# Performance work log

Hardware: AMD Instinct MI355X
Metric: run time of the kernel (lower is better)

## Reference

```python
import jax, jax.numpy as jnp
import numpy as np

N_CHILDS = 50000
N_EDGES = 500000
NODE_FEAT = 256
NUM_SEM = 57
HID = 256
EDGE_FEAT = 64
EDGE_TYPES = 4
NUM_ITERS = 2


def setup_inputs() -> dict:
    key = jax.random.key(0)
    ks = jax.random.split(key, 12)
    d_in = NODE_FEAT + NUM_SEM            # 313
    d_ne = 2 * HID + EDGE_FEAT + EDGE_TYPES  # 580
    d_par = HID * (NUM_ITERS + 1)         # 768
    def lin(k, fan_in, fan_out):
        kw, kb = jax.random.split(k)
        s = 1.0 / np.sqrt(fan_in)
        return (jax.random.uniform(kw, (fan_in, fan_out), jnp.float32, -s, s),
                jax.random.uniform(kb, (fan_out,), jnp.float32, -s, s))
    W_child, b_child = lin(ks[0], d_in, HID)
    W_ne0, b_ne0 = lin(ks[1], d_ne, HID)
    W_ne1, b_ne1 = lin(ks[2], d_ne, HID)
    W_parent, b_parent = lin(ks[3], d_par, NODE_FEAT)
    return {
        "child_feats": jax.random.normal(ks[4], (1, N_CHILDS, d_in), jnp.float32),
        "child_exists": jnp.ones((1, N_CHILDS, 1), jnp.float32),
        "edge_type_onehot": jax.random.normal(ks[5], (1, N_EDGES, EDGE_TYPES), jnp.float32),
        "edge_feats": jax.random.normal(ks[6], (1, N_EDGES, EDGE_FEAT), jnp.float32),
        "edge_indices": jax.random.randint(ks[7], (1, N_EDGES, 2), 0, N_CHILDS, jnp.int64),
        "W_child": W_child, "b_child": b_child,
        "W_ne0": W_ne0, "b_ne0": b_ne0,
        "W_ne1": W_ne1, "b_ne1": b_ne1,
        "W_parent": W_parent, "b_parent": b_parent,
    }


def reference(child_feats, child_exists, edge_type_onehot, edge_feats, edge_indices,
              W_child, b_child, W_ne0, b_ne0, W_ne1, b_ne1, W_parent, b_parent):
    n = child_feats.shape[1]
    # node embedding: linear + relu, mask non-existent children
    x = jax.nn.relu(jnp.einsum('bnd,dh->bnh', child_feats, W_child) + b_child)
    x = x * child_exists                              # [1, N, H]
    iter_parent = [x.max(axis=1)]                     # symmetric_type == 'max'
    ef = jnp.concatenate([edge_type_onehot, edge_feats], axis=2)[0]  # [E, 4+64]
    src = edge_indices[0, :, 0]
    dst = edge_indices[0, :, 1]
    cnt = jax.ops.segment_sum(jnp.ones((src.shape[0],), x.dtype), src, num_segments=n)
    denom = jnp.maximum(cnt, 1.0)[:, None]            # scatter_mean clamp
    for W, b in ((W_ne0, b_ne0), (W_ne1, b_ne1)):
        nef = jnp.concatenate([x[0, src], x[0, dst], ef], axis=1)  # [E, 580]
        nef = jax.nn.relu(nef @ W + b)                # [E, H]
        # edge_symmetric_type == 'avg': scatter_mean over source index
        x = (jax.ops.segment_sum(nef, src, num_segments=n) / denom)[None]
        iter_parent.append(x.max(axis=1))
    parent = jnp.concatenate(iter_parent, axis=1)     # [1, H*(iters+1)]
    return jax.nn.relu(parent @ W_parent + b_parent)  # [1, node_feat_size]
```

## Files before the change

### kernel.cpp

```cpp
#include <hip/hip_runtime.h>

#define NC   50000
#define NE   500000
#define NEP  (NE + 64)
#define DIN  313
#define DNE  580
#define KPC  320
#define KB   96
#define NB_SCAN 196

typedef __attribute__((ext_vector_type(8))) short bf16x8;
typedef __attribute__((ext_vector_type(4))) float f32x4;

static __device__ __forceinline__ unsigned short f2bf(float f) {
    unsigned u = __float_as_uint(f);
    unsigned r = (u + 0x7fff + ((u >> 16) & 1)) >> 16;
    return (unsigned short)r;
}
static __device__ __forceinline__ float bf2f(unsigned short u) {
    return __uint_as_float(((unsigned)u) << 16);
}
static __device__ __forceinline__ void gload_lds16(const unsigned short* g, unsigned short* l) {
    __builtin_amdgcn_global_load_lds(
        (const __attribute__((address_space(1))) unsigned int*)(g),
        (__attribute__((address_space(3))) unsigned int*)(l), 16, 0, 0);
}

__global__ __launch_bounds__(256) void prep_w_kernel(
    const float* __restrict__ W0, const float* __restrict__ W1,
    const float* __restrict__ Wc,
    unsigned short* __restrict__ Wpt, unsigned short* __restrict__ Wbt,
    unsigned short* __restrict__ Wct)
{
    int b = blockIdx.x;
    if (b < 1024) {
        int layer = b >> 9, n2 = b & 511;
        const float* W = layer ? W1 : W0;
        unsigned short* dst = Wpt + (size_t)layer * 512 * 256 + (size_t)n2 * 256;
        int t = threadIdx.x;
        int ch = t >> 5, s = (t >> 3) & 3, j = t & 7;
        int gk = ch * 32 + ((s ^ (n2 & 3)) * 8) + j;
        float v = (n2 < 256) ? W[(size_t)gk * 256 + n2] : W[(size_t)(256 + gk) * 256 + (n2 - 256)];
        dst[t] = f2bf(v);
    } else if (b < 1536) {
        int idx = b - 1024;
        int layer = idx >> 8, n = idx & 255;
        const float* W = layer ? W1 : W0;
        unsigned short* dst = Wbt + (size_t)layer * 256 * KB + (size_t)n * KB;
        int t = threadIdx.x;
        if (t < KB) {
            int ch = t >> 5, s = (t >> 3) & 3, j = t & 7;
            int gk = ch * 32 + ((s ^ (n & 3)) * 8) + j;
            float v = (512 + gk < DNE) ? W[(size_t)(512 + gk) * 256 + n] : 0.0f;
            dst[t] = f2bf(v);
        }
    } else {
        int n = b - 1536;
        unsigned short* dst = Wct + (size_t)n * KPC;
        for (int t = threadIdx.x; t < KPC; t += 256) {
            int ch = t >> 5, s = (t >> 3) & 3, j = t & 7;
            int gk = ch * 32 + ((s ^ (n & 3)) * 8) + j;
            float v = (gk < DIN) ? Wc[(size_t)gk * 256 + n] : 0.0f;
            dst[t] = f2bf(v);
        }
    }
}

__global__ __launch_bounds__(256, 4) void child_mfma_kernel(
    const float* __restrict__ cf, const float* __restrict__ exists,
    const unsigned short* __restrict__ Wct, const float* __restrict__ bias,
    unsigned short* __restrict__ xb, float* __restrict__ pmax)
{
    __shared__ unsigned short sA[64][40];
    __shared__ unsigned short sB[256][32];
    __shared__ float smax[256];

    const int tid = threadIdx.x, lane = tid & 63, wid = tid >> 6;
    const int wm = wid >> 1, wn = wid & 1, l15 = lane & 15, l4 = lane >> 4;
    const int node0 = blockIdx.x * 64;
    const int arow = tid >> 2, s3 = tid & 3;

    smax[tid] = 0.0f;

    f32x4 acc[2][8];
    #pragma unroll
    for (int mi = 0; mi < 2; ++mi)
        #pragma unroll
        for (int ni = 0; ni < 8; ++ni)
            acc[mi][ni] = (f32x4){0.f, 0.f, 0.f, 0.f};

    int nodeA = node0 + arow; if (nodeA >= NC) nodeA = NC - 1;

    for (int ch = 0; ch < 10; ++ch) {
        #pragma unroll
        for (int i = 0; i < 4; ++i) {
            int n = (wid << 6) + (i << 4) + (lane >> 2);
            gload_lds16(Wct + (size_t)n * KPC + ch * 32 + (lane & 3) * 8,
                        &sB[(wid << 6) + (i << 4)][0]);
        }
        {
            int gk0 = ch * 32 + s3 * 8;
            union { unsigned short u[8]; int4 v; } pk;
            #pragma unroll
            for (int j = 0; j < 8; ++j) {
                int gk = gk0 + j;
                float f = (gk < DIN) ? cf[(size_t)nodeA * DIN + gk] : 0.0f;
                pk.u[j] = f2bf(f);
            }
            *(int4*)&sA[arow][s3 * 8] = pk.v;
        }
        __syncthreads();
        bf16x8 af[2];
        #pragma unroll
        for (int mi = 0; mi < 2; ++mi)
            af[mi] = *(const bf16x8*)&sA[wm * 32 + mi * 16 + l15][l4 * 8];
        #pragma unroll
        for (int ni = 0; ni < 8; ++ni) {
            int n = wn * 128 + ni * 16 + l15;
            bf16x8 bfr = *(const bf16x8*)&sB[n][(l4 ^ (n & 3)) * 8];
            acc[0][ni] = __builtin_amdgcn_mfma_f32_16x16x32_bf16(af[0], bfr, acc[0][ni], 0, 0, 0);
            acc[1][ni] = __builtin_amdgcn_mfma_f32_16x16x32_bf16(af[1], bfr, acc[1][ni], 0, 0, 0);
        }
        __syncthreads();
    }

    float bv[8];
    #pragma unroll
    for (int ni = 0; ni < 8; ++ni) bv[ni] = bias[wn * 128 + ni * 16 + l15];
    float cmax[8];
    #pragma unroll
    for (int ni = 0; ni < 8; ++ni) cmax[ni] = 0.0f;

    #pragma unroll
    for (int mi = 0; mi < 2; ++mi) {
        #pragma unroll
        for (int r = 0; r < 4; ++r) {
            int node = node0 + wm * 32 + mi * 16 + l4 * 4 + r;
            if (node < NC) {
                float ex = exists[node];
                #pragma unroll
                for (int ni = 0; ni < 8; ++ni) {
                    float v = fmaxf(acc[mi][ni][r] + bv[ni], 0.f) * ex;
                    xb[(size_t)node * 256 + wn * 128 + ni * 16 + l15] = f2bf(v);
                    cmax[ni] = fmaxf(cmax[ni], v);
                }
            }
        }
    }
    #pragma unroll
    for (int ni = 0; ni < 8; ++ni)
        atomicMax((unsigned int*)&smax[wn * 128 + ni * 16 + l15], __float_as_uint(cmax[ni]));
    __syncthreads();
    atomicMax((unsigned int*)&pmax[tid], __float_as_uint(smax[tid]));
}

__global__ __launch_bounds__(256, 3) void node_gemm_kernel(
    const unsigned short* __restrict__ xb,
    const unsigned short* __restrict__ Wpt,
    unsigned short* __restrict__ yp)
{
    __shared__ unsigned short sA[2][64][40];
    __shared__ unsigned short sB[2][256][32];

    const int tid = threadIdx.x, lane = tid & 63, wid = tid >> 6;
    const int wm = wid >> 1, wn = wid & 1, l15 = lane & 15, l4 = lane >> 4;
    const int node0 = blockIdx.x * 64;
    const int n0 = blockIdx.y * 256;
    const int arow = tid >> 2, s3 = tid & 3;

    int nodeA = node0 + arow; if (nodeA >= NC) nodeA = NC - 1;

    f32x4 acc[2][8];
    #pragma unroll
    for (int mi = 0; mi < 2; ++mi)
        #pragma unroll
        for (int ni = 0; ni < 8; ++ni)
            acc[mi][ni] = (f32x4){0.f, 0.f, 0.f, 0.f};

    #pragma unroll
    for (int i = 0; i < 4; ++i) {
        int n = (wid << 6) + (i << 4) + (lane >> 2);
        gload_lds16(Wpt + (size_t)(n0 + n) * 256 + (lane & 3) * 8, &sB[0][(wid << 6) + (i << 4)][0]);
    }
    *(int4*)&sA[0][arow][s3 * 8] = *(const int4*)(xb + (size_t)nodeA * 256 + s3 * 8);
    __syncthreads();

    int buf = 0;
    for (int ch = 0; ch < 8; ++ch) {
        const int nch = ch + 1;
        int4 areg;
        if (nch < 8) {
            #pragma unroll
            for (int i = 0; i < 4; ++i) {
                int n = (wid << 6) + (i << 4) + (lane >> 2);
                gload_lds16(Wpt + (size_t)(n0 + n) * 256 + nch * 32 + (lane & 3) * 8,
                            &sB[buf ^ 1][(wid << 6) + (i << 4)][0]);
            }
            areg = *(const int4*)(xb + (size_t)nodeA * 256 + nch * 32 + s3 * 8);
        }
        bf16x8 af[2];
        #pragma unroll
        for (int mi = 0; mi < 2; ++mi)
            af[mi] = *(const bf16x8*)&sA[buf][wm * 32 + mi * 16 + l15][l4 * 8];
        #pragma unroll
        for (int ni = 0; ni < 8; ++ni) {
            int n = wn * 128 + ni * 16 + l15;
            bf16x8 bfr = *(const bf16x8*)&sB[buf][n][(l4 ^ (n & 3)) * 8];
            acc[0][ni] = __builtin_amdgcn_mfma_f32_16x16x32_bf16(af[0], bfr, acc[0][ni], 0, 0, 0);
            acc[1][ni] = __builtin_amdgcn_mfma_f32_16x16x32_bf16(af[1], bfr, acc[1][ni], 0, 0, 0);
        }
        if (nch < 8) *(int4*)&sA[buf ^ 1][arow][s3 * 8] = areg;
        __syncthreads();
        buf ^= 1;
    }

    #pragma unroll
    for (int mi = 0; mi < 2; ++mi) {
        #pragma unroll
        for (int r = 0; r < 4; ++r) {
            int node = node0 + wm * 32 + mi * 16 + l4 * 4 + r;
            if (node < NC) {
                #pragma unroll
                for (int ni = 0; ni < 8; ++ni)
                    yp[(size_t)node * 512 + n0 + wn * 128 + ni * 16 + l15] = f2bf(acc[mi][ni][r]);
            }
        }
    }
}

__global__ __launch_bounds__(256) void count_int_kernel(
    const int* __restrict__ eidx, int* __restrict__ icnt)
{
    int t = blockIdx.x * 256 + threadIdx.x;
    if (t < NE) atomicAdd(&icnt[eidx[2 * t]], 1);
}

__global__ __launch_bounds__(256) void scan1_kernel(
    const int* __restrict__ icnt, int* __restrict__ part)
{
    __shared__ int sd[256];
    int i = blockIdx.x * 256 + threadIdx.x;
    sd[threadIdx.x] = (i < NC) ? icnt[i] : 0;
    __syncthreads();
    for (int d = 128; d > 0; d >>= 1) {
        if (threadIdx.x < d) sd[threadIdx.x] += sd[threadIdx.x + d];
        __syncthreads();
    }
    if (threadIdx.x == 0) part[blockIdx.x] = sd[0];
}

__global__ void scan2_kernel(int* __restrict__ part)
{
    if (threadIdx.x == 0) {
        int acc = 0;
        for (int i = 0; i < NB_SCAN; ++i) { int v = part[i]; part[i] = acc; acc += v; }
    }
}

__global__ __launch_bounds__(256) void scan3_kernel(
    const int* __restrict__ icnt, const int* __restrict__ part,
    int* __restrict__ cur)
{
    __shared__ int sc[256];
    const int t = threadIdx.x;
    int i = blockIdx.x * 256 + t;
    int val = (i < NC) ? icnt[i] : 0;
    sc[t] = val;
    __syncthreads();
    for (int d = 1; d < 256; d <<= 1) {
        int x = (t >= d) ? sc[t - d] : 0;
        __syncthreads();
        sc[t] += x;
        __syncthreads();
    }
    if (i < NC) cur[i] = part[blockIdx.x] + sc[t] - val;
}

__global__ __launch_bounds__(256) void bin_kernel(
    const int* __restrict__ eidx, int* __restrict__ cur, int* __restrict__ perm)
{
    int t = blockIdx.x * 256 + threadIdx.x;
    if (t < NE) {
        int s = eidx[2 * t];
        int p = atomicAdd(&cur[s], 1);
        perm[p] = t;
    }
}

__global__ __launch_bounds__(256) void inv_kernel(
    const int* __restrict__ icnt, float* __restrict__ inv)
{
    int t = blockIdx.x * 256 + threadIdx.x;
    if (t < NC) inv[t] = 1.0f / fmaxf((float)icnt[t], 1.0f);
}

__global__ __launch_bounds__(256) void ef_prep_kernel(
    const float* __restrict__ eto, const float* __restrict__ efe,
    const int* __restrict__ perm, const int* __restrict__ eidx,
    unsigned short* __restrict__ efc01, unsigned short* __restrict__ efc2,
    int* __restrict__ esrc, int* __restrict__ edst)
{
    int p = blockIdx.x * 256 + threadIdx.x;
    if (p >= NE) return;
    int e = perm[p];
    esrc[p] = eidx[2 * e];
    edst[p] = eidx[2 * e + 1];
    const float* efr = efe + (size_t)e * 64;

    union { unsigned short u[8]; int4 v; } pk;
    {
        float4 a = *(const float4*)(eto + (size_t)e * 4);
        float4 b = *(const float4*)(efr + 0);
        pk.u[0]=f2bf(a.x); pk.u[1]=f2bf(a.y); pk.u[2]=f2bf(a.z); pk.u[3]=f2bf(a.w);
        pk.u[4]=f2bf(b.x); pk.u[5]=f2bf(b.y); pk.u[6]=f2bf(b.z); pk.u[7]=f2bf(b.w);
        *(int4*)(efc01 + (size_t)p * 32) = pk.v;
    }
    #pragma unroll
    for (int g = 1; g < 4; ++g) {
        float4 a = *(const float4*)(efr + g * 8 - 4);
        float4 b = *(const float4*)(efr + g * 8);
        pk.u[0]=f2bf(a.x); pk.u[1]=f2bf(a.y); pk.u[2]=f2bf(a.z); pk.u[3]=f2bf(a.w);
        pk.u[4]=f2bf(b.x); pk.u[5]=f2bf(b.y); pk.u[6]=f2bf(b.z); pk.u[7]=f2bf(b.w);
        *(int4*)(efc01 + (size_t)p * 32 + g * 8) = pk.v;
    }
    #pragma unroll
    for (int g = 0; g < 4; ++g) {
        float4 a = *(const float4*)(efr + 28 + g * 8);
        float4 b = *(const float4*)(efr + 32 + g * 8);
        pk.u[0]=f2bf(a.x); pk.u[1]=f2bf(a.y); pk.u[2]=f2bf(a.z); pk.u[3]=f2bf(a.w);
        pk.u[4]=f2bf(b.x); pk.u[5]=f2bf(b.y); pk.u[6]=f2bf(b.z); pk.u[7]=f2bf(b.w);
        *(int4*)(efc01 + ((size_t)NEP + p) * 32 + g * 8) = pk.v;
    }
    {
        float4 a = *(const float4*)(efr + 60);
        pk.u[0]=f2bf(a.x); pk.u[1]=f2bf(a.y); pk.u[2]=f2bf(a.z); pk.u[3]=f2bf(a.w);
        pk.u[4]=0; pk.u[5]=0; pk.u[6]=0; pk.u[7]=0;
        *(int4*)(efc2 + (size_t)p * 8) = pk.v;
    }
}

__global__ __launch_bounds__(256, 3) void combine_efc_kernel(
    const unsigned short* __restrict__ yp,
    const unsigned short* __restrict__ efc01,
    const unsigned short* __restrict__ efc2,
    const int* __restrict__ esrc, const int* __restrict__ edst,
    const unsigned short* __restrict__ Wbt,
    const float* __restrict__ bias,
    float* __restrict__ accb)
{
    __shared__ __align__(16) unsigned char smem[25600];
    unsigned short (*sA01)[64][32] = (unsigned short (*)[64][32])(smem);
    unsigned short (*sA2)[8]       = (unsigned short (*)[8])(smem + 8192);
    unsigned short (*sW)[32]       = (unsigned short (*)[32])(smem + 9216);
    float (*ep)[258]               = (float (*)[258])(smem);
    __shared__ int s_src[64], s_dst[64];

    const int tid = threadIdx.x;
    const int nwg = gridDim.x;
    const int q = nwg >> 3, rr = nwg & 7;
    const int xcd = blockIdx.x & 7, within = blockIdx.x >> 3;
    const int bid = (xcd < rr ? xcd * (q + 1) : rr * (q + 1) + (xcd - rr) * q) + within;
    const int e0 = bid * 64;

    const int lane = tid & 63;
    const int wid  = tid >> 6;
    const int wm   = wid >> 1;
    const int wn   = wid & 1;
    const int l15  = lane & 15;
    const int l4   = lane >> 4;

    if (tid < 64) {
        int e = e0 + tid; if (e > NE - 1) e = NE - 1;
        s_src[tid] = esrc[e];
        s_dst[tid] = edst[e];
    }
    gload_lds16(efc01 + ((size_t)e0 + wid * 16) * 32 + lane * 8, &sA01[0][wid * 16][0]);
    gload_lds16(efc01 + ((size_t)NEP + e0 + wid * 16) * 32 + lane * 8, &sA01[1][wid * 16][0]);
    if (wid == 0)
        gload_lds16(efc2 + (size_t)e0 * 8 + lane * 8, &sA2[0][0]);
    #pragma unroll
    for (int i = 0; i < 4; ++i) {
        gload_lds16(Wbt + (size_t)((wid << 6) + (i << 4) + (lane >> 2)) * KB + (lane & 3) * 8,
                    &sW[(wid << 6) + (i << 4)][0]);
    }
    __syncthreads();

    f32x4 acc[2][8];
    #pragma unroll
    for (int mi = 0; mi < 2; ++mi)
        #pragma unroll
        for (int ni = 0; ni < 8; ++ni)
            acc[mi][ni] = (f32x4){0.f, 0.f, 0.f, 0.f};

    #pragma unroll
    for (int ch = 0; ch < 3; ++ch) {
        if (ch > 0) {
            __syncthreads();
            #pragma unroll
            for (int i = 0; i < 4; ++i) {
                gload_lds16(Wbt + (size_t)((wid << 6) + (i << 4) + (lane >> 2)) * KB + ch * 32 + (lane & 3) * 8,
                            &sW[(wid << 6) + (i << 4)][0]);
            }
            __syncthreads();
        }
        bf16x8 af0, af1;
        if (ch < 2) {
            af0 = *(const bf16x8*)&sA01[ch][wm * 32 + l15][l4 * 8];
            af1 = *(const bf16x8*)&sA01[ch][wm * 32 + 16 + l15][l4 * 8];
        } else {
            bf16x8 z = (bf16x8){0,0,0,0,0,0,0,0};
            bf16x8 a0 = *(const bf16x8*)&sA2[wm * 32 + l15][0];
            bf16x8 a1 = *(const bf16x8*)&sA2[wm * 32 + 16 + l15][0];
            af0 = (l4 == 0) ? a0 : z;
            af1 = (l4 == 0) ? a1 : z;
        }
        #pragma unroll
        for (int ni = 0; ni < 8; ++ni) {
            int n = wn * 128 + ni * 16 + l15;
            bf16x8 bfr = *(const bf16x8*)&sW[n][(l4 ^ (n & 3)) * 8];
            acc[0][ni] = __builtin_amdgcn_mfma_f32_16x16x32_bf16(af0, bfr, acc[0][ni], 0, 0, 0);
            acc[1][ni] = __builtin_amdgcn_mfma_f32_16x16x32_bf16(af1, bfr, acc[1][ni], 0, 0, 0);
        }
    }
    __syncthreads();

    const int col = tid;
    const float b_col = bias[col];

    int curn = s_src[0];
    int rstart = 0;
    float run = 0.f;
    #pragma unroll
    for (int c = 0; c < 4; ++c) {
        if (wm == (c >> 1)) {
            const int mi = c & 1;
            #pragma unroll
            for (int ni = 0; ni < 8; ++ni) {
                #pragma unroll
                for (int r = 0; r < 4; ++r)
                    ep[l4 * 4 + r][wn * 128 + ni * 16 + l15] = acc[mi][ni][r];
            }
        }
        float yt[16], ym[16];
        #pragma unroll
        for (int r = 0; r < 16; ++r) {
            int row = c * 16 + r;
            yt[r] = bf2f(yp[(size_t)s_src[row] * 512 + col]);
            ym[r] = bf2f(yp[(size_t)s_dst[row] * 512 + 256 + col]);
        }
        __syncthreads();
        #pragma unroll
        for (int r = 0; r < 16; ++r) {
            int row = c * 16 + r;
            float v = 0.0f;
            if (e0 + row < NE)
                v = fmaxf(ep[r][col] + yt[r] + ym[r] + b_col, 0.f);
            int sr = s_src[row];
            if (sr != curn) {
                if (rstart > 0) accb[(size_t)curn * 256 + col] = run;
                else            atomicAdd(&accb[(size_t)curn * 256 + col], run);
                curn = sr; run = v; rstart = row;
            } else {
                run += v;
            }
        }
        __syncthreads();
    }
    atomicAdd(&accb[(size_t)curn * 256 + col], run);
}

__global__ __launch_bounds__(256, 3) void combine_f32_kernel(
    const unsigned short* __restrict__ yp,
    const float* __restrict__ eto, const float* __restrict__ efe,
    const int* __restrict__ eidx, const int* __restrict__ perm,
    const unsigned short* __restrict__ Wbt,
    const float* __restrict__ bias,
    float* __restrict__ accb)
{
    __shared__ unsigned short sA[3][64][40];
    __shared__ unsigned short sW[2][256][32];
    __shared__ int s_src[64], s_dst[64], s_perm[64];

    const int tid = threadIdx.x;
    const int nwg = gridDim.x;
    const int q = nwg >> 3, rr = nwg & 7;
    const int xcd = blockIdx.x & 7, within = blockIdx.x >> 3;
    const int bid = (xcd < rr ? xcd * (q + 1) : rr * (q + 1) + (xcd - rr) * q) + within;
    const int e0 = bid * 64;

    if (tid < 64) {
        int ee = e0 + tid; if (ee >= NE) ee = NE - 1;
        int e = perm[ee];
        s_perm[tid] = e;
        s_src[tid] = eidx[2 * e];
        s_dst[tid] = eidx[2 * e + 1];
    }
    const int lane = tid & 63;
    const int wid  = tid >> 6;
    const int wm   = wid >> 1;
    const int wn   = wid & 1;
    const int l15  = lane & 15;
    const int l4   = lane >> 4;
    const int arow = tid >> 2;
    const int s3   = tid & 3;

    f32x4 acc[2][8];
    #pragma unroll
    for (int mi = 0; mi < 2; ++mi)
        #pragma unroll
        for (int ni = 0; ni < 8; ++ni)
            acc[mi][ni] = (f32x4){0.f, 0.f, 0.f, 0.f};

    #pragma unroll
    for (int i = 0; i < 4; ++i) {
        int n = (wid << 6) + (i << 4) + (lane >> 2);
        gload_lds16(Wbt + (size_t)n * KB + (lane & 3) * 8, &sW[0][(wid << 6) + (i << 4)][0]);
    }
    __syncthreads();

    const int my_e = s_perm[arow];
    #pragma unroll
    for (int ch = 0; ch < 3; ++ch) {
        int g0 = ch * 32 + s3 * 8;
        union { unsigned short u[8]; int4 v; } pk;
        #pragma unroll
        for (int j = 0; j < 8; ++j) {
            int g = g0 + j;
            float f = 0.0f;
            if (g < 4)       f = eto[(size_t)my_e * 4 + g];
            else if (g < 68) f = efe[(size_t)my_e * 64 + (g - 4)];
            pk.u[j] = f2bf(f);
        }
        *(int4*)&sA[ch][arow][s3 * 8] = pk.v;
    }
    __syncthreads();

    int buf = 0;
    #pragma unroll
    for (int ch = 0; ch < 3; ++ch) {
        if (ch + 1 < 3) {
            #pragma unroll
            for (int i = 0; i < 4; ++i) {
                int n = (wid << 6) + (i << 4) + (lane >> 2);
                gload_lds16(Wbt + (size_t)n * KB + (ch + 1) * 32 + (lane & 3) * 8,
                            &sW[buf ^ 1][(wid << 6) + (i << 4)][0]);
            }
        }
        bf16x8 af[2];
        #pragma unroll
        for (int mi = 0; mi < 2; ++mi)
            af[mi] = *(const bf16x8*)&sA[ch][wm * 32 + mi * 16 + l15][l4 * 8];
        #pragma unroll
        for (int ni = 0; ni < 8; ++ni) {
            int n = wn * 128 + ni * 16 + l15;
            bf16x8 bfr = *(const bf16x8*)&sW[buf][n][(l4 ^ (n & 3)) * 8];
            acc[0][ni] = __builtin_amdgcn_mfma_f32_16x16x32_bf16(af[0], bfr, acc[0][ni], 0, 0, 0);
            acc[1][ni] = __builtin_amdgcn_mfma_f32_16x16x32_bf16(af[1], bfr, acc[1][ni], 0, 0, 0);
        }
        __syncthreads();
        buf ^= 1;
    }

    float (*ep)[258] = (float (*)[258])(&sW[0][0][0]);
    const int col = tid;
    const float b_col = bias[col];

    int curn = s_src[0];
    int rstart = 0;
    float run = 0.f;
    #pragma unroll
    for (int c = 0; c < 4; ++c) {
        if (wm == (c >> 1)) {
            const int mi = c & 1;
            #pragma unroll
            for (int ni = 0; ni < 8; ++ni) {
                #pragma unroll
                for (int r = 0; r < 4; ++r)
                    ep[l4 * 4 + r][wn * 128 + ni * 16 + l15] = acc[mi][ni][r];
            }
        }
        float yt[16], ym[16];
        #pragma unroll
        for (int r = 0; r < 16; ++r) {
            int row = c * 16 + r;
            yt[r] = bf2f(yp[(size_t)s_src[row] * 512 + col]);
            ym[r] = bf2f(yp[(size_t)s_dst[row] * 512 + 256 + col]);
        }
        __syncthreads();
        #pragma unroll
        for (int r = 0; r < 16; ++r) {
            int row = c * 16 + r;
            float v = 0.0f;
            if (e0 + row < NE)
                v = fmaxf(ep[r][col] + yt[r] + ym[r] + b_col, 0.f);
            int sr = s_src[row];
            if (sr != curn) {
                if (rstart > 0) accb[(size_t)curn * 256 + col] = run;
                else            atomicAdd(&accb[(size_t)curn * 256 + col], run);
                curn = sr; run = v; rstart = row;
            } else {
                run += v;
            }
        }
        __syncthreads();
    }
    atomicAdd(&accb[(size_t)curn * 256 + col], run);
}

__global__ __launch_bounds__(256) void finalize_kernel(
    const float* __restrict__ src, const float* __restrict__ inv,
    unsigned short* __restrict__ xb_out, float* __restrict__ pmax, int n)
{
    const int tid = threadIdx.x;
    int i0 = blockIdx.x * 128;
    int iend = i0 + 128; if (iend > n) iend = n;
    float m = 0.0f;
    for (int i = i0; i < iend; ++i) {
        float v = src[(size_t)i * 256 + tid];
        v *= inv[i];
        xb_out[(size_t)i * 256 + tid] = f2bf(v);
        m = fmaxf(m, v);
    }
    atomicMax((unsigned int*)&pmax[tid], __float_as_uint(m));
}

__global__ __launch_bounds__(256) void parent_kernel(
    const float* __restrict__ pmax, const float* __restrict__ W,
    const float* __restrict__ bias, float* __restrict__ out)
{
    __shared__ float sp[768];
    const int tid = threadIdx.x;
    for (int i = tid; i < 768; i += 256) sp[i] = pmax[i];
    __syncthreads();
    float s = bias[tid];
    for (int k = 0; k < 768; ++k) s = fmaf(sp[k], W[(size_t)k * 256 + tid], s);
    out[tid] = fmaxf(s, 0.f);
}

extern "C" void kernel_launch(void* const* d_in, const int* in_sizes, int n_in,
                              void* d_out, int out_size, void* d_ws, size_t ws_size,
                              hipStream_t stream)
{
    const float* cf   = (const float*)d_in[0];
    const float* ex   = (const float*)d_in[1];
    const float* eto  = (const float*)d_in[2];
    const float* efe  = (const float*)d_in[3];
    const int*   eidx = (const int*)d_in[4];
    const float* Wc   = (const float*)d_in[5];
    const float* bc   = (const float*)d_in[6];
    const float* W0   = (const float*)d_in[7];
    const float* b0   = (const float*)d_in[8];
    const float* W1   = (const float*)d_in[9];
    const float* b1   = (const float*)d_in[10];
    const float* Wp   = (const float*)d_in[11];
    const float* bp   = (const float*)d_in[12];

    float*          accb = (float*)d_ws;
    float*          invv = accb + (size_t)NC * 256;
    float*          pmax = invv + NC;
    unsigned short* xb   = (unsigned short*)(pmax + 768);
    unsigned short* yp   = xb + (size_t)NC * 256;
    unsigned short* Wpt  = yp + (size_t)NC * 512;
    unsigned short* Wbt  = Wpt + (size_t)2 * 512 * 256;
    unsigned short* Wct  = Wbt + (size_t)2 * 256 * KB;
    int*            icnt = (int*)(Wct + (size_t)256 * KPC);
    int*            part = icnt + NC;
    int*            curb = part + 256;
    int*            perm = curb + NC;
    unsigned short* efc01 = (unsigned short*)(perm + NE);
    unsigned short* efc2  = efc01 + (size_t)2 * NEP * 32;
    int*            esrc  = (int*)(efc2 + (size_t)NEP * 8);
    int*            edst  = esrc + NE;
    size_t need = (size_t)((char*)(edst + NE) - (char*)d_ws);
    const bool use_efc = (ws_size >= need);

    hipMemsetAsync(pmax, 0, 768 * sizeof(float), stream);
    hipMemsetAsync(icnt, 0, NC * sizeof(int), stream);

    prep_w_kernel<<<1792, 256, 0, stream>>>(W0, W1, Wc, Wpt, Wbt, Wct);
    child_mfma_kernel<<<(NC + 63) / 64, 256, 0, stream>>>(cf, ex, Wct, bc, xb, pmax);

    count_int_kernel<<<(NE + 255) / 256, 256, 0, stream>>>(eidx, icnt);
    scan1_kernel<<<NB_SCAN, 256, 0, stream>>>(icnt, part);
    scan2_kernel<<<1, 64, 0, stream>>>(part);
    scan3_kernel<<<NB_SCAN, 256, 0, stream>>>(icnt, part, curb);
    bin_kernel<<<(NE + 255) / 256, 256, 0, stream>>>(eidx, curb, perm);
    inv_kernel<<<(NC + 255) / 256, 256, 0, stream>>>(icnt, invv);
    if (use_efc)
        ef_prep_kernel<<<(NE + 255) / 256, 256, 0, stream>>>(eto, efe, perm, eidx, efc01, efc2, esrc, edst);

    const int nwg = (NE + 63) / 64;
    for (int it = 0; it < 2; ++it) {
        node_gemm_kernel<<<dim3((NC + 63) / 64, 2), 256, 0, stream>>>(
            xb, Wpt + (size_t)it * 512 * 256, yp);
        hipMemsetAsync(accb, 0, (size_t)NC * 256 * sizeof(float), stream);
        if (use_efc)
            combine_efc_kernel<<<nwg, 256, 0, stream>>>(
                yp, efc01, efc2, esrc, edst,
                Wbt + (size_t)it * 256 * KB, it ? b1 : b0, accb);
        else
            combine_f32_kernel<<<nwg, 256, 0, stream>>>(
                yp, eto, efe, eidx, perm,
                Wbt + (size_t)it * 256 * KB, it ? b1 : b0, accb);
        finalize_kernel<<<(NC + 127) / 128, 256, 0, stream>>>(accb, invv, xb, pmax + 256 * (it + 1), NC);
    }
    parent_kernel<<<1, 256, 0, stream>>>(pmax, Wp, bp, (float*)d_out);
}
```

Baseline: 729.7 us.

## Split edge combine kernel across two column halves to raise occupancy

The edge combine kernel now launches a 2D grid where each block handles 128 of the 256 output columns, which halves the accumulator registers, the weight tile and the epilogue shared buffer. Launch bounds rise from 3 to 8 blocks per SIMD group. The epilogue now splits the 64 edge rows into two 32-row groups handled by separate thread halves, each with its own run-length segment reduce and atomic boundaries. The aim is higher occupancy to hide the gather latency of yp. The cost is that edge features and indices are loaded twice, and segment boundaries produce more atomics.

```diff
diff --git a/kernel.cpp b/kernel.cpp
--- a/kernel.cpp
+++ b/kernel.cpp
@@ -339,7 +339,7 @@
     }
 }
 
-__global__ __launch_bounds__(256, 3) void combine_efc_kernel(
+__global__ __launch_bounds__(256, 8) void combine_efc_kernel(
     const unsigned short* __restrict__ yp,
     const unsigned short* __restrict__ efc01,
     const unsigned short* __restrict__ efc2,
@@ -348,26 +348,24 @@
     const float* __restrict__ bias,
     float* __restrict__ accb)
 {
-    __shared__ __align__(16) unsigned char smem[25600];
+    __shared__ __align__(16) unsigned char smem[17408];
     unsigned short (*sA01)[64][32] = (unsigned short (*)[64][32])(smem);
     unsigned short (*sA2)[8]       = (unsigned short (*)[8])(smem + 8192);
     unsigned short (*sW)[32]       = (unsigned short (*)[32])(smem + 9216);
-    float (*ep)[258]               = (float (*)[258])(smem);
+    float (*ep)[132]               = (float (*)[132])(smem);
     __shared__ int s_src[64], s_dst[64];
 
     const int tid = threadIdx.x;
     const int nwg = gridDim.x;
     const int q = nwg >> 3, rr = nwg & 7;
     const int xcd = blockIdx.x & 7, within = blockIdx.x >> 3;
-    const int bid = (xcd < rr ? xcd * (q + 1) : rr * (q + 1) + (xcd - rr) * q) + within;
-    const int e0 = bid * 64;
-
-    const int lane = tid & 63;
-    const int wid  = tid >> 6;
-    const int wm   = wid >> 1;
-    const int wn   = wid & 1;
-    const int l15  = lane & 15;
-    const int l4   = lane >> 4;
+    const int ebid = (xcd < rr ? xcd * (q + 1) : rr * (q + 1) + (xcd - rr) * q) + within;
+    const int e0 = ebid * 64;
+    const int ncol0 = blockIdx.y * 128;
+
+    const int lane = tid & 63, wid = tid >> 6;
+    const int l15 = lane & 15, l4 = lane >> 4;
+    const int lc = tid & 127, rg = tid >> 7;
 
     if (tid < 64) {
         int e = e0 + tid; if (e > NE - 1) e = NE - 1;
@@ -379,89 +377,92 @@
     if (wid == 0)
         gload_lds16(efc2 + (size_t)e0 * 8 + lane * 8, &sA2[0][0]);
     #pragma unroll
-    for (int i = 0; i < 4; ++i) {
-        gload_lds16(Wbt + (size_t)((wid << 6) + (i << 4) + (lane >> 2)) * KB + (lane & 3) * 8,
-                    &sW[(wid << 6) + (i << 4)][0]);
-    }
-    __syncthreads();
-
-    f32x4 acc[2][8];
-    #pragma unroll
-    for (int mi = 0; mi < 2; ++mi)
-        #pragma unroll
-        for (int ni = 0; ni < 8; ++ni)
-            acc[mi][ni] = (f32x4){0.f, 0.f, 0.f, 0.f};
+    for (int i = 0; i < 2; ++i) {
+        int rowW = (wid << 5) + (i << 4);
+        gload_lds16(Wbt + (size_t)(ncol0 + rowW + (lane >> 2)) * KB + (lane & 3) * 8,
+                    &sW[rowW][0]);
+    }
+    __syncthreads();
+
+    f32x4 acc[8];
+    #pragma unroll
+    for (int ni = 0; ni < 8; ++ni)
+        acc[ni] = (f32x4){0.f, 0.f, 0.f, 0.f};
 
     #pragma unroll
     for (int ch = 0; ch < 3; ++ch) {
         if (ch > 0) {
             __syncthreads();
             #pragma unroll
-            for (int i = 0; i < 4; ++i) {
-                gload_lds16(Wbt + (size_t)((wid << 6) + (i << 4) + (lane >> 2)) * KB + ch * 32 + (lane & 3) * 8,
-                            &sW[(wid << 6) + (i << 4)][0]);
+            for (int i = 0; i < 2; ++i) {
+                int rowW = (wid << 5) + (i << 4);
+                gload_lds16(Wbt + (size_t)(ncol0 + rowW + (lane >> 2)) * KB + ch * 32 + (lane & 3) * 8,
+                            &sW[rowW][0]);
             }
             __syncthreads();
         }
-        bf16x8 af0, af1;
+        bf16x8 af;
         if (ch < 2) {
-            af0 = *(const bf16x8*)&sA01[ch][wm * 32 + l15][l4 * 8];
-            af1 = *(const bf16x8*)&sA01[ch][wm * 32 + 16 + l15][l4 * 8];
+            af = *(const bf16x8*)&sA01[ch][wid * 16 + l15][l4 * 8];
         } else {
             bf16x8 z = (bf16x8){0,0,0,0,0,0,0,0};
-            bf16x8 a0 = *(const bf16x8*)&sA2[wm * 32 + l15][0];
-            bf16x8 a1 = *(const bf16x8*)&sA2[wm * 32 + 16 + l15][0];
-            af0 = (l4 == 0) ? a0 : z;
-            af1 = (l4 == 0) ? a1 : z;
+            bf16x8 a0 = *(const bf16x8*)&sA2[wid * 16 + l15][0];
+            af = (l4 == 0) ? a0 : z;
         }
         #pragma unroll
         for (int ni = 0; ni < 8; ++ni) {
-            int n = wn * 128 + ni * 16 + l15;
+            int n = ni * 16 + l15;
             bf16x8 bfr = *(const bf16x8*)&sW[n][(l4 ^ (n & 3)) * 8];
-            acc[0][ni] = __builtin_amdgcn_mfma_f32_16x16x32_bf16(af0, bfr, acc[0][ni], 0, 0, 0);
-            acc[1][ni] = __builtin_amdgcn_mfma_f32_16x16x32_bf16(af1, bfr, acc[1][ni], 0, 0, 0);
-        }
-    }
-    __syncthreads();
-
-    const int col = tid;
+            acc[ni] = __builtin_amdgcn_mfma_f32_16x16x32_bf16(af, bfr, acc[ni], 0, 0, 0);
+        }
+    }
+    __syncthreads();
+
+    const int col = ncol0 + lc;
     const float b_col = bias[col];
-
-    int curn = s_src[0];
-    int rstart = 0;
+    const int gstart = rg << 5;
+    int curn = s_src[gstart];
+    int rstart = gstart;
     float run = 0.f;
+
     #pragma unroll
     for (int c = 0; c < 4; ++c) {
-        if (wm == (c >> 1)) {
-            const int mi = c & 1;
+        if (wid == c) {
             #pragma unroll
             for (int ni = 0; ni < 8; ++ni) {
                 #pragma unroll
                 for (int r = 0; r < 4; ++r)
-                    ep[l4 * 4 + r][wn * 128 + ni * 16 + l15] = acc[mi][ni][r];
-            }
-        }
-        float yt[16], ym[16];
-        #pragma unroll
-        for (int r = 0; r < 16; ++r) {
-            int row = c * 16 + r;
-            yt[r] = bf2f(yp[(size_t)s_src[row] * 512 + col]);
-            ym[r] = bf2f(yp[(size_t)s_dst[row] * 512 + 256 + col]);
-        }
-        __syncthreads();
-        #pragma unroll
-        for (int r = 0; r < 16; ++r) {
-            int row = c * 16 + r;
-            float v = 0.0f;
-            if (e0 + row < NE)
-                v = fmaxf(ep[r][col] + yt[r] + ym[r] + b_col, 0.f);
-            int sr = s_src[row];
-            if (sr != curn) {
-                if (rstart > 0) accb[(size_t)curn * 256 + col] = run;
-                else            atomicAdd(&accb[(size_t)curn * 256 + col], run);
-                curn = sr; run = v; rstart = row;
-            } else {
-                run += v;
+                    ep[l4 * 4 + r][ni * 16 + l15] = acc[ni][r];
+            }
+        }
+        __syncthreads();
+        if (rg == (c >> 1)) {
+            #pragma unroll
+            for (int sb = 0; sb < 2; ++sb) {
+                float yt[8], ym[8];
+                #pragma unroll
+                for (int r = 0; r < 8; ++r) {
+                    int row = c * 16 + sb * 8 + r;
+                    unsigned so = ((unsigned)s_src[row] << 9) + (unsigned)col;
+                    unsigned dofs = ((unsigned)s_dst[row] << 9) + 256u + (unsigned)col;
+                    yt[r] = bf2f(yp[so]);
+                    ym[r] = bf2f(yp[dofs]);
+                }
+                #pragma unroll
+                for (int r = 0; r < 8; ++r) {
+                    int row = c * 16 + sb * 8 + r;
+                    float v = 0.0f;
+                    if (e0 + row < NE)
+                        v = fmaxf(ep[sb * 8 + r][lc] + yt[r] + ym[r] + b_col, 0.f);
+                    int sr = s_src[row];
+                    if (sr != curn) {
+                        if (rstart > gstart) accb[(size_t)curn * 256 + col] = run;
+                        else                 atomicAdd(&accb[(size_t)curn * 256 + col], run);
+                        curn = sr; run = v; rstart = row;
+                    } else {
+                        run += v;
+                    }
+                }
             }
         }
         __syncthreads();
@@ -695,7 +696,7 @@
             xb, Wpt + (size_t)it * 512 * 256, yp);
         hipMemsetAsync(accb, 0, (size_t)NC * 256 * sizeof(float), stream);
         if (use_efc)
-            combine_efc_kernel<<<nwg, 256, 0, stream>>>(
+            combine_efc_kernel<<<dim3(nwg, 2), 256, 0, stream>>>(
                 yp, efc01, efc2, esrc, edst,
                 Wbt + (size_t)it * 256 * KB, it ? b1 : b0, accb);
         else
```

Result: slower. 857.7 us (+17.5%).

## Stage whole edge tile as bf16 in LDS and double-buffer gather loads

Applied to the files above, without the earlier changes.

The combine epilogue now writes the full 64x256 MFMA result tile to LDS once, as bf16 in a larger shared buffer, instead of four fp32 16-row passes with two barriers each. The gathered yp rows are loaded in two register banks, so the next 16-row chunk's gather is issued while the current chunk is reduced. Launch bounds rise from 3 to 4 blocks per CU. The aim is fewer barriers and more latency hiding for the random gathers. In exchange the MFMA output is rounded to bf16 before the bias and ReLU, the LDS footprint grows, and register pressure rises.

```diff
diff --git a/kernel.cpp b/kernel.cpp
--- a/kernel.cpp
+++ b/kernel.cpp
@@ -339,7 +339,32 @@
     }
 }
 
-__global__ __launch_bounds__(256, 3) void combine_efc_kernel(
+#define LOAD16(B, YT, YM)                                              \
+    _Pragma("unroll")                                                  \
+    for (int r = 0; r < 16; ++r) {                                     \
+        int row = (B) * 16 + r;                                        \
+        YT[r] = bf2f(yp[((unsigned)s_src[row] << 9) + (unsigned)col]); \
+        YM[r] = bf2f(yp[((unsigned)s_dst[row] << 9) + 256u + (unsigned)col]); \
+    }
+
+#define WALK16(B, YT, YM)                                              \
+    _Pragma("unroll")                                                  \
+    for (int r = 0; r < 16; ++r) {                                     \
+        int row = (B) * 16 + r;                                        \
+        float v = 0.0f;                                                \
+        if (e0 + row < NE)                                             \
+            v = fmaxf(bf2f(epb[row][col]) + YT[r] + YM[r] + b_col, 0.f); \
+        int sr = s_src[row];                                           \
+        if (sr != curn) {                                              \
+            if (rstart > 0) accb[(size_t)curn * 256 + col] = run;      \
+            else            atomicAdd(&accb[(size_t)curn * 256 + col], run); \
+            curn = sr; run = v; rstart = row;                          \
+        } else {                                                       \
+            run += v;                                                  \
+        }                                                              \
+    }
+
+__global__ __launch_bounds__(256, 4) void combine_efc_kernel(
     const unsigned short* __restrict__ yp,
     const unsigned short* __restrict__ efc01,
     const unsigned short* __restrict__ efc2,
@@ -348,11 +373,11 @@
     const float* __restrict__ bias,
     float* __restrict__ accb)
 {
-    __shared__ __align__(16) unsigned char smem[25600];
+    __shared__ __align__(16) unsigned char smem[34816];
     unsigned short (*sA01)[64][32] = (unsigned short (*)[64][32])(smem);
     unsigned short (*sA2)[8]       = (unsigned short (*)[8])(smem + 8192);
     unsigned short (*sW)[32]       = (unsigned short (*)[32])(smem + 9216);
-    float (*ep)[258]               = (float (*)[258])(smem);
+    unsigned short (*epb)[272]     = (unsigned short (*)[272])(smem);
     __shared__ int s_src[64], s_dst[64];
 
     const int tid = threadIdx.x;
@@ -424,48 +449,32 @@
     }
     __syncthreads();
 
+    #pragma unroll
+    for (int mi = 0; mi < 2; ++mi)
+        #pragma unroll
+        for (int ni = 0; ni < 8; ++ni)
+            #pragma unroll
+            for (int r = 0; r < 4; ++r)
+                epb[wm * 32 + mi * 16 + l4 * 4 + r][wn * 128 + ni * 16 + l15] = f2bf(acc[mi][ni][r]);
+
     const int col = tid;
     const float b_col = bias[col];
+    float ytA[16], ymA[16], ytB[16], ymB[16];
+    LOAD16(0, ytA, ymA)
+    LOAD16(1, ytB, ymB)
+    __syncthreads();
 
     int curn = s_src[0];
     int rstart = 0;
     float run = 0.f;
-    #pragma unroll
-    for (int c = 0; c < 4; ++c) {
-        if (wm == (c >> 1)) {
-            const int mi = c & 1;
-            #pragma unroll
-            for (int ni = 0; ni < 8; ++ni) {
-                #pragma unroll
-                for (int r = 0; r < 4; ++r)
-                    ep[l4 * 4 + r][wn * 128 + ni * 16 + l15] = acc[mi][ni][r];
-            }
-        }
-        float yt[16], ym[16];
-        #pragma unroll
-        for (int r = 0; r < 16; ++r) {
-            int row = c * 16 + r;
-            yt[r] = bf2f(yp[(size_t)s_src[row] * 512 + col]);
-            ym[r] = bf2f(yp[(size_t)s_dst[row] * 512 + 256 + col]);
-        }
-        __syncthreads();
-        #pragma unroll
-        for (int r = 0; r < 16; ++r) {
-            int row = c * 16 + r;
-            float v = 0.0f;
-            if (e0 + row < NE)
-                v = fmaxf(ep[r][col] + yt[r] + ym[r] + b_col, 0.f);
-            int sr = s_src[row];
-            if (sr != curn) {
-                if (rstart > 0) accb[(size_t)curn * 256 + col] = run;
-                else            atomicAdd(&accb[(size_t)curn * 256 + col], run);
-                curn = sr; run = v; rstart = row;
-            } else {
-                run += v;
-            }
-        }
-        __syncthreads();
-    }
+
+    WALK16(0, ytA, ymA)
+    LOAD16(2, ytA, ymA)
+    WALK16(1, ytB, ymB)
+    LOAD16(3, ytB, ymB)
+    WALK16(2, ytA, ymA)
+    WALK16(3, ytB, ymB)
+
     atomicAdd(&accb[(size_t)curn * 256 + col], run);
 }
 
```

Result: faster. 624.7 us (-14.4%).
